# Optimization experiments

Hardware: AMD Instinct MI355X
Metric: run time of the kernel (lower is better)

The kernel has to match this reference:

```python
import jax, jax.numpy as jnp
import numpy as np

B, C, H, W, K = 2, 64, 192, 192, 7
PAD = K // 2
EPS = 1e-6


def _win_idx(L):
    # NATTEN border handling: window is shifted (not zero-padded) to stay in-bounds.
    i = jnp.arange(L)
    start = jnp.clip(i - PAD, 0, L - K)            # [L] window start per query pos
    win = start[:, None] + jnp.arange(K)[None]     # [L,K] absolute key positions
    pb = (K - 1) - (i - start)                     # [L] rpb start index per query pos
    pbi = pb[:, None] + jnp.arange(K)[None]        # [L,K] rpb table indices
    return win, pbi


def setup_inputs() -> dict:
    key = jax.random.key(0)
    ks = jax.random.split(key, 10)
    g = jax.random.normal(ks[0], (B, C, H, W), jnp.float32)
    cd = jax.random.uniform(ks[1], (B, 1, H, W), dtype=jnp.float32)
    dense = jax.random.uniform(ks[2], (B, 1, H, W), dtype=jnp.float32)
    sel = jax.random.uniform(ks[3], (B, 1, H, W)) < 0.05
    sd = jnp.where(sel, dense, 0.0)
    mask = (jax.random.uniform(ks[4], (B, 1, H, W)) < 0.5).astype(jnp.float32)
    ln_w = 1.0 + 0.02 * jax.random.normal(ks[5], (C,), jnp.float32)
    ln_b = 0.02 * jax.random.normal(ks[6], (C,), jnp.float32)
    conv_w = 0.05 * jax.random.normal(ks[7], (2 * C, C + 1), jnp.float32)  # 1x1 conv
    conv_b = 0.02 * jax.random.normal(ks[8], (2 * C,), jnp.float32)
    rpb = 0.02 * jax.random.normal(ks[9], (1, 2 * K - 1, 2 * K - 1), jnp.float32)
    return {"g": g, "cd": cd, "sd": sd, "mask": mask,
            "ln_w": ln_w, "ln_b": ln_b, "conv_w": conv_w, "conv_b": conv_b, "rpb": rpb}


def reference(g, cd, sd, mask, ln_w, ln_b, conv_w, conv_b, rpb):
    # LayerNorm2d: normalize over channel dim per spatial location
    mu = g.mean(axis=1, keepdims=True)
    var = ((g - mu) ** 2).mean(axis=1, keepdims=True)
    gn = (g - mu) * jax.lax.rsqrt(var + EPS)
    gn = gn * ln_w[None, :, None, None] + ln_b[None, :, None, None]

    z = jnp.concatenate([gn, cd], axis=1)                      # [B,C+1,H,W]
    qk = jnp.einsum('bchw,oc->bohw', z, conv_w) + conv_b[None, :, None, None]
    q, k = qk[:, :C], qk[:, C:]
    k = k * mask

    qc = q.transpose(0, 2, 3, 1)                               # [B,H,W,C] single head
    kc = k.transpose(0, 2, 3, 1)
    rwin, rpbi = _win_idx(H)
    cwin, cpbi = _win_idx(W)

    # NATTEN qk + relative position bias over 7x7 neighborhoods
    k_win = kc[:, rwin][:, :, :, cwin]                         # [B,H,K,W,K,C]
    attn = jnp.einsum('bhwc,bhiwjc->bhwij', qc, k_win)         # [B,H,W,K,K]
    bias = rpb[0][rpbi][:, :, cpbi]                            # [H,K,W,K]
    attn = attn + bias.transpose(0, 2, 1, 3)[None]
    a = jax.nn.softmax(attn.reshape(B, H, W, K * K), axis=-1).reshape(B, H, W, K, K)

    # NATTEN av with v = cd (head_dim 1)
    v_win = cd[:, 0][:, rwin][:, :, :, cwin]                   # [B,H,K,W,K]
    cd_out = jnp.einsum('bhwij,bhiwj->bhw', a, v_win)[:, None]  # [B,1,H,W]
    m_win = mask[:, 0][:, rwin][:, :, :, cwin]
    mask_out = jnp.einsum('bhwij,bhiwj->bhw', a, m_win)[:, None]

    # NYU / SDR post-processing
    cd_out = cd_out * mask + cd * (1.0 - mask)
    valid = sd > 0
    cd_out = jnp.where(valid, sd, cd_out)
    mask_out = jnp.where(valid, mask, mask_out)
    return cd_out, mask_out
```

## Files before the change

kernel.cpp:

```cpp
#include <hip/hip_runtime.h>

constexpr int NB = 2;
constexpr int NC = 64;
constexpr int NH = 192;
constexpr int NW = 192;
constexpr int NK = 7;
constexpr int NHW = NH * NW;
constexpr int NPIX = NB * NHW;
constexpr float EPS = 1e-6f;

__global__ __launch_bounds__(256) void qk_gemm(
    const float* __restrict__ g, const float* __restrict__ cd,
    const float* __restrict__ mask,
    const float* __restrict__ ln_w, const float* __restrict__ ln_b,
    const float* __restrict__ conv_w, const float* __restrict__ conv_b,
    float* __restrict__ qbuf, float* __restrict__ kbuf)
{
    __shared__ float Z[65][128];
    __shared__ float WTc[33][128];

    int tid = threadIdx.x;
    int p0 = blockIdx.x * 128;
    int b  = p0 / NHW;
    int hw0 = p0 - b * NHW;

    int px = tid >> 1;
    int hf = tid & 1;
    const float* gp = g + (size_t)(b * NC + hf * 32) * NHW + (hw0 + px);
    float vals[32];
    float s = 0.f, sq = 0.f;
#pragma unroll
    for (int j = 0; j < 32; ++j) {
        float v = gp[(size_t)j * NHW];
        vals[j] = v; s += v; sq += v * v;
    }
    s  += __shfl_xor(s, 1);
    sq += __shfl_xor(sq, 1);
    float mu   = s * (1.f / 64.f);
    float rstd = rsqrtf(sq * (1.f / 64.f) - mu * mu + EPS);
#pragma unroll
    for (int j = 0; j < 32; ++j) {
        int c = hf * 32 + j;
        Z[c][px] = (vals[j] - mu) * rstd * ln_w[c] + ln_b[c];
    }
    if (hf) Z[64][px] = cd[p0 + px];

    int og = tid >> 4;
    int pg = tid & 15;
    float acc[8][8];
#pragma unroll
    for (int oi = 0; oi < 8; ++oi)
#pragma unroll
        for (int pj = 0; pj < 8; ++pj) acc[oi][pj] = 0.f;

    for (int cc = 0; cc < 65; cc += 33) {
        int nr = (65 - cc < 33) ? (65 - cc) : 33;
        __syncthreads();
        if (tid < 128) {
            int o = tid;
            for (int r = 0; r < nr; ++r)
                WTc[r][o] = conv_w[o * 65 + cc + r];
        }
        __syncthreads();
        for (int r = 0; r < nr; ++r) {
            float4 w0 = *(const float4*)&WTc[r][8 * og];
            float4 w1 = *(const float4*)&WTc[r][8 * og + 4];
            float4 z0 = *(const float4*)&Z[cc + r][8 * pg];
            float4 z1 = *(const float4*)&Z[cc + r][8 * pg + 4];
            float w8[8] = {w0.x, w0.y, w0.z, w0.w, w1.x, w1.y, w1.z, w1.w};
            float z8[8] = {z0.x, z0.y, z0.z, z0.w, z1.x, z1.y, z1.z, z1.w};
#pragma unroll
            for (int oi = 0; oi < 8; ++oi)
#pragma unroll
                for (int pj = 0; pj < 8; ++pj)
                    acc[oi][pj] = fmaf(w8[oi], z8[pj], acc[oi][pj]);
        }
    }

    int o0  = og * 8;
    int pxb = pg * 8;
    float4 ba = *(const float4*)&conv_b[o0];
    float4 bb = *(const float4*)&conv_b[o0 + 4];
    float bia[8] = {ba.x, ba.y, ba.z, ba.w, bb.x, bb.y, bb.z, bb.w};
    bool isq = (o0 < 64);
    float m8[8];
    if (!isq) {
        float4 ma = *(const float4*)&mask[p0 + pxb];
        float4 mc = *(const float4*)&mask[p0 + pxb + 4];
        m8[0]=ma.x; m8[1]=ma.y; m8[2]=ma.z; m8[3]=ma.w;
        m8[4]=mc.x; m8[5]=mc.y; m8[6]=mc.z; m8[7]=mc.w;
    }
    float* base = isq ? (qbuf + (size_t)(b * NC + o0) * NHW + hw0 + pxb)
                      : (kbuf + (size_t)(b * NC + o0 - 64) * NHW + hw0 + pxb);
#pragma unroll
    for (int oi = 0; oi < 8; ++oi) {
        float v[8];
#pragma unroll
        for (int pj = 0; pj < 8; ++pj) {
            float t = acc[oi][pj] + bia[oi];
            v[pj] = isq ? t : t * m8[pj];
        }
        float* dst = base + (size_t)oi * NHW;
        *(float4*)&dst[0] = make_float4(v[0], v[1], v[2], v[3]);
        *(float4*)&dst[4] = make_float4(v[4], v[5], v[6], v[7]);
    }
}

__global__ __launch_bounds__(256) void attn_tile(
    const float* __restrict__ qbuf, const float* __restrict__ kbuf,
    const float* __restrict__ cd, const float* __restrict__ sd,
    const float* __restrict__ mask, const float* __restrict__ rpb,
    float* __restrict__ out_cd, float* __restrict__ out_mask)
{
    __shared__ float kst[4][2][10 * 24];
    __shared__ float cdt[14 * 24];
    __shared__ float mt [14 * 24];
    __shared__ float rpbt[169];
    __shared__ float xch[128][49];

    int tid  = threadIdx.x;
    int g    = tid >> 6;
    int lane = tid & 63;
    int rq   = g & 1;
    int half = g >> 1;
    int tx   = lane & 15;
    int tyw  = lane >> 4;

    int bw = blockIdx.x % 12;
    int t2 = blockIdx.x / 12;
    int bh = t2 % 24;
    int b  = t2 / 24;
    int w0 = bw * 16, h0 = bh * 8;
    int hr0 = h0 + rq * 4;

    int h = hr0 + tyw;
    int w = w0 + tx;
    int rs = min(max(h - 3, 0), NH - NK);
    int cs = min(max(w - 3, 0), NW - NK);
    int rb  = (rs - (hr0 - 3)) * 24 + (cs - (w0 - 3));
    int rbB = (rs - (h0  - 3)) * 24 + (cs - (w0 - 3));

    const float* cdb = cd   + (size_t)b * NHW;
    const float* msb = mask + (size_t)b * NHW;
    for (int e = tid; e < 308; e += 256) {
        int r = e / 22, c2 = e - r * 22;
        int gr = min(max(h0 - 3 + r, 0), NH - 1);
        int gc = min(max(w0 - 3 + c2, 0), NW - 1);
        cdt[r * 24 + c2] = cdb[gr * NW + gc];
        mt [r * 24 + c2] = msb[gr * NW + gc];
    }
    if (tid < 169) rpbt[tid] = rpb[tid];

    int soff[4], slds[4]; bool sact[4];
#pragma unroll
    for (int s = 0; s < 4; ++s) {
        int e = lane + 64 * s;
        int r = e / 22, c2 = e - r * 22;
        int gr = min(max(hr0 - 3 + r, 0), NH - 1);
        int gc = min(max(w0 - 3 + c2, 0), NW - 1);
        soff[s] = gr * NW + gc;
        slds[s] = r * 24 + c2;
        sact[s] = (e < 220);
    }

    const float* kb = kbuf + (size_t)(b * NC + half * 32) * NHW;
    const float* qb = qbuf + (size_t)(b * NC + half * 32) * NHW + h * NW + w;

    float at[49];
#pragma unroll
    for (int n = 0; n < 49; ++n) at[n] = 0.f;

    float st[4];
#pragma unroll
    for (int s = 0; s < 4; ++s) st[s] = sact[s] ? kb[soff[s]] : 0.f;
    float* k0 = kst[g][0];
    float* k1 = kst[g][1];
#pragma unroll
    for (int s = 0; s < 4; ++s) if (sact[s]) k0[slds[s]] = st[s];

    for (int i = 0; i < 32; ++i) {
        if (i + 1 < 32) {
            const float* kb2 = kb + (size_t)(i + 1) * NHW;
#pragma unroll
            for (int s = 0; s < 4; ++s) st[s] = sact[s] ? kb2[soff[s]] : 0.f;
        }
        float q = qb[(size_t)i * NHW];
        const float* kt = ((i & 1) ? k1 : k0) + rb;
#pragma unroll
        for (int r = 0; r < 7; ++r)
#pragma unroll
            for (int j = 0; j < 7; ++j)
                at[r * 7 + j] = fmaf(q, kt[r * 24 + j], at[r * 7 + j]);
        if (i + 1 < 32) {
            float* nk = (i & 1) ? k0 : k1;
#pragma unroll
            for (int s = 0; s < 4; ++s) if (sact[s]) nk[slds[s]] = st[s];
        }
    }

    int pxid = (rq * 4 + tyw) * 16 + tx;
    __syncthreads();
    if (half == 1) {
#pragma unroll
        for (int n = 0; n < 49; ++n) xch[pxid][n] = at[n];
    }
    __syncthreads();
    int pr = 6 - (h - rs);
    int pc = 6 - (w - cs);
    if (half == 0) {
#pragma unroll
        for (int n = 0; n < 49; ++n) at[n] += xch[pxid][n];
#pragma unroll
        for (int r = 0; r < 7; ++r)
#pragma unroll
            for (int j = 0; j < 7; ++j)
                at[r * 7 + j] += rpbt[(pr + r) * 13 + pc + j];
#pragma unroll
        for (int n = 0; n < 49; ++n) xch[pxid][n] = at[n];
    }
    __syncthreads();
    if (half == 1) {
#pragma unroll
        for (int n = 0; n < 49; ++n) at[n] = xch[pxid][n];
    }

    float mx = -1e30f;
#pragma unroll
    for (int n = 0; n < 49; ++n) mx = fmaxf(mx, at[n]);
    float sm = 0.f;
#pragma unroll
    for (int n = 0; n < 49; ++n) {
        at[n] = __expf(at[n] - mx);
        sm += at[n];
    }

    const float* vt = (half ? mt : cdt) + rbB;
    float sv = 0.f;
#pragma unroll
    for (int r = 0; r < 7; ++r)
#pragma unroll
        for (int j = 0; j < 7; ++j)
            sv = fmaf(at[r * 7 + j], vt[r * 24 + j], sv);
    sv /= sm;

    int p = b * NHW + h * NW + w;
    float sdc = sd[p];
    int cidx = (rq * 4 + tyw + 3) * 24 + (tx + 3);
    float mc = mt[cidx];
    if (half == 0) {
        float cdc = cdt[cidx];
        float co = sv * mc + cdc * (1.f - mc);
        if (sdc > 0.f) co = sdc;
        out_cd[p] = co;
    } else {
        out_mask[p] = (sdc > 0.f) ? mc : sv;
    }
}

extern "C" void kernel_launch(void* const* d_in, const int* in_sizes, int n_in,
                              void* d_out, int out_size, void* d_ws, size_t ws_size,
                              hipStream_t stream) {
    const float* g      = (const float*)d_in[0];
    const float* cd     = (const float*)d_in[1];
    const float* sd     = (const float*)d_in[2];
    const float* mask   = (const float*)d_in[3];
    const float* ln_w   = (const float*)d_in[4];
    const float* ln_b   = (const float*)d_in[5];
    const float* conv_w = (const float*)d_in[6];
    const float* conv_b = (const float*)d_in[7];
    const float* rpb    = (const float*)d_in[8];

    float* out  = (float*)d_out;
    float* qbuf = (float*)d_ws;
    float* kbuf = qbuf + (size_t)NB * NC * NHW;

    qk_gemm<<<dim3(NPIX / 128), dim3(256), 0, stream>>>(
        g, cd, mask, ln_w, ln_b, conv_w, conv_b, qbuf, kbuf);
    attn_tile<<<dim3(NB * 24 * 12), dim3(256), 0, stream>>>(
        qbuf, kbuf, cd, sd, mask, rpb, out, out + NPIX);
}
```

Before: 141.7 us.

## Interleave q/k channels in groups of four and load float4 in attention

```diff
diff --git a/kernel.cpp b/kernel.cpp
--- a/kernel.cpp
+++ b/kernel.cpp
@@ -9,12 +9,13 @@
 constexpr int NPIX = NB * NHW;
 constexpr float EPS = 1e-6f;
 
+
 __global__ __launch_bounds__(256) void qk_gemm(
     const float* __restrict__ g, const float* __restrict__ cd,
     const float* __restrict__ mask,
     const float* __restrict__ ln_w, const float* __restrict__ ln_b,
     const float* __restrict__ conv_w, const float* __restrict__ conv_b,
-    float* __restrict__ qbuf, float* __restrict__ kbuf)
+    float* __restrict__ qk)
 {
     __shared__ float Z[65][128];
     __shared__ float WTc[33][128];
@@ -90,33 +91,33 @@
         m8[0]=ma.x; m8[1]=ma.y; m8[2]=ma.z; m8[3]=ma.w;
         m8[4]=mc.x; m8[5]=mc.y; m8[6]=mc.z; m8[7]=mc.w;
     }
-    float* base = isq ? (qbuf + (size_t)(b * NC + o0) * NHW + hw0 + pxb)
-                      : (kbuf + (size_t)(b * NC + o0 - 64) * NHW + hw0 + pxb);
-#pragma unroll
-    for (int oi = 0; oi < 8; ++oi) {
-        float v[8];
+#pragma unroll
+    for (int qd = 0; qd < 2; ++qd) {
+        int grp = (o0 >> 2) + qd;
+        float* dst = qk + ((size_t)(b * 32 + grp) * NHW + hw0 + pxb) * 4;
 #pragma unroll
         for (int pj = 0; pj < 8; ++pj) {
-            float t = acc[oi][pj] + bia[oi];
-            v[pj] = isq ? t : t * m8[pj];
-        }
-        float* dst = base + (size_t)oi * NHW;
-        *(float4*)&dst[0] = make_float4(v[0], v[1], v[2], v[3]);
-        *(float4*)&dst[4] = make_float4(v[4], v[5], v[6], v[7]);
+            float vv[4];
+#pragma unroll
+            for (int ci = 0; ci < 4; ++ci) {
+                float tv = acc[qd * 4 + ci][pj] + bia[qd * 4 + ci];
+                vv[ci] = isq ? tv : tv * m8[pj];
+            }
+            *(float4*)(dst + pj * 4) = make_float4(vv[0], vv[1], vv[2], vv[3]);
+        }
     }
 }
 
 __global__ __launch_bounds__(256) void attn_tile(
-    const float* __restrict__ qbuf, const float* __restrict__ kbuf,
+    const float* __restrict__ qk,
     const float* __restrict__ cd, const float* __restrict__ sd,
     const float* __restrict__ mask, const float* __restrict__ rpb,
     float* __restrict__ out_cd, float* __restrict__ out_mask)
 {
-    __shared__ float kst[4][2][10 * 24];
-    __shared__ float cdt[14 * 24];
-    __shared__ float mt [14 * 24];
-    __shared__ float rpbt[169];
-    __shared__ float xch[128][49];
+    __shared__ float smem[7680 + 336 + 336 + 169];
+    float* cdt  = smem + 7680;
+    float* mt   = smem + 7680 + 336;
+    float* rpbt = smem + 7680 + 672;
 
     int tid  = threadIdx.x;
     int g    = tid >> 6;
@@ -126,8 +127,10 @@
     int tx   = lane & 15;
     int tyw  = lane >> 4;
 
-    int bw = blockIdx.x % 12;
-    int t2 = blockIdx.x / 12;
+    int bid = blockIdx.x;
+    int swz = (bid & 7) * 72 + (bid >> 3);
+    int bw = swz % 12;
+    int t2 = swz / 12;
     int bh = t2 % 24;
     int b  = t2 / 24;
     int w0 = bw * 16, h0 = bh * 8;
@@ -158,46 +161,69 @@
         int r = e / 22, c2 = e - r * 22;
         int gr = min(max(hr0 - 3 + r, 0), NH - 1);
         int gc = min(max(w0 - 3 + c2, 0), NW - 1);
-        soff[s] = gr * NW + gc;
+        soff[s] = (gr * NW + gc) * 4;
         slds[s] = r * 24 + c2;
         sact[s] = (e < 220);
     }
 
-    const float* kb = kbuf + (size_t)(b * NC + half * 32) * NHW;
-    const float* qb = qbuf + (size_t)(b * NC + half * 32) * NHW + h * NW + w;
+    const float* kb0 = qk + (size_t)(b * 32 + 16 + half * 8) * NHW * 4;
+    const float* qb0 = qk + ((size_t)(b * 32 + half * 8) * NHW + h * NW + w) * 4;
+
+    float* kw = smem + g * 1920;
 
     float at[49];
 #pragma unroll
     for (int n = 0; n < 49; ++n) at[n] = 0.f;
 
-    float st[4];
-#pragma unroll
-    for (int s = 0; s < 4; ++s) st[s] = sact[s] ? kb[soff[s]] : 0.f;
-    float* k0 = kst[g][0];
-    float* k1 = kst[g][1];
-#pragma unroll
-    for (int s = 0; s < 4; ++s) if (sact[s]) k0[slds[s]] = st[s];
-
-    for (int i = 0; i < 32; ++i) {
-        if (i + 1 < 32) {
-            const float* kb2 = kb + (size_t)(i + 1) * NHW;
-#pragma unroll
-            for (int s = 0; s < 4; ++s) st[s] = sact[s] ? kb2[soff[s]] : 0.f;
-        }
-        float q = qb[(size_t)i * NHW];
-        const float* kt = ((i & 1) ? k1 : k0) + rb;
-#pragma unroll
-        for (int r = 0; r < 7; ++r)
-#pragma unroll
-            for (int j = 0; j < 7; ++j)
-                at[r * 7 + j] = fmaf(q, kt[r * 24 + j], at[r * 7 + j]);
-        if (i + 1 < 32) {
-            float* nk = (i & 1) ? k0 : k1;
-#pragma unroll
-            for (int s = 0; s < 4; ++s) if (sact[s]) nk[slds[s]] = st[s];
-        }
-    }
-
+    float4 stg[4];
+    float4 qn;
+#pragma unroll
+    for (int s = 0; s < 4; ++s)
+        stg[s] = sact[s] ? *(const float4*)(kb0 + soff[s])
+                         : make_float4(0.f, 0.f, 0.f, 0.f);
+    qn = *(const float4*)qb0;
+#pragma unroll
+    for (int s = 0; s < 4; ++s) if (sact[s]) {
+        kw[0 * 240 + slds[s]] = stg[s].x;
+        kw[1 * 240 + slds[s]] = stg[s].y;
+        kw[2 * 240 + slds[s]] = stg[s].z;
+        kw[3 * 240 + slds[s]] = stg[s].w;
+    }
+
+    for (int t = 0; t < 8; ++t) {
+        float4 qv = qn;
+        if (t < 7) {
+            const float* kbn = kb0 + (size_t)(t + 1) * (NHW * 4);
+#pragma unroll
+            for (int s = 0; s < 4; ++s)
+                if (sact[s]) stg[s] = *(const float4*)(kbn + soff[s]);
+            qn = *(const float4*)(qb0 + (size_t)(t + 1) * (NHW * 4));
+        }
+        const float* kbuf = kw + (t & 1) * 960;
+#pragma unroll
+        for (int ccq = 0; ccq < 4; ++ccq) {
+            float q = (ccq == 0) ? qv.x : (ccq == 1) ? qv.y
+                    : (ccq == 2) ? qv.z : qv.w;
+            const float* kt = kbuf + ccq * 240 + rb;
+#pragma unroll
+            for (int r = 0; r < 7; ++r)
+#pragma unroll
+                for (int j = 0; j < 7; ++j)
+                    at[r * 7 + j] = fmaf(q, kt[r * 24 + j], at[r * 7 + j]);
+        }
+        if (t < 7) {
+            float* nk = kw + ((t + 1) & 1) * 960;
+#pragma unroll
+            for (int s = 0; s < 4; ++s) if (sact[s]) {
+                nk[0 * 240 + slds[s]] = stg[s].x;
+                nk[1 * 240 + slds[s]] = stg[s].y;
+                nk[2 * 240 + slds[s]] = stg[s].z;
+                nk[3 * 240 + slds[s]] = stg[s].w;
+            }
+        }
+    }
+
+    float (*xch)[49] = (float(*)[49])smem;
     int pxid = (rq * 4 + tyw) * 16 + tx;
     __syncthreads();
     if (half == 1) {
@@ -270,12 +296,11 @@
     const float* conv_b = (const float*)d_in[7];
     const float* rpb    = (const float*)d_in[8];
 
-    float* out  = (float*)d_out;
-    float* qbuf = (float*)d_ws;
-    float* kbuf = qbuf + (size_t)NB * NC * NHW;
+    float* out   = (float*)d_out;
+    float* qkbuf = (float*)d_ws;
 
     qk_gemm<<<dim3(NPIX / 128), dim3(256), 0, stream>>>(
-        g, cd, mask, ln_w, ln_b, conv_w, conv_b, qbuf, kbuf);
+        g, cd, mask, ln_w, ln_b, conv_w, conv_b, qkbuf);
     attn_tile<<<dim3(NB * 24 * 12), dim3(256), 0, stream>>>(
-        qbuf, kbuf, cd, sd, mask, rpb, out, out + NPIX);
+        qkbuf, cd, sd, mask, rpb, out, out + NPIX);
 }
```

After: 158.0 us. 1.12x slower.

## Deepen K-channel prefetch to 4-stage LDS ring and swizzle block order

Applied to the files above, without the earlier changes.

```diff
diff --git a/kernel.cpp b/kernel.cpp
--- a/kernel.cpp
+++ b/kernel.cpp
@@ -112,7 +112,7 @@
     const float* __restrict__ mask, const float* __restrict__ rpb,
     float* __restrict__ out_cd, float* __restrict__ out_mask)
 {
-    __shared__ float kst[4][2][10 * 24];
+    __shared__ float kst[4][4][240];
     __shared__ float cdt[14 * 24];
     __shared__ float mt [14 * 24];
     __shared__ float rpbt[169];
@@ -126,8 +126,10 @@
     int tx   = lane & 15;
     int tyw  = lane >> 4;
 
-    int bw = blockIdx.x % 12;
-    int t2 = blockIdx.x / 12;
+    int bid = blockIdx.x;
+    int swz = (bid & 7) * 72 + (bid >> 3);
+    int bw = swz % 12;
+    int t2 = swz / 12;
     int bh = t2 % 24;
     int b  = t2 / 24;
     int w0 = bw * 16, h0 = bh * 8;
@@ -170,32 +172,48 @@
 #pragma unroll
     for (int n = 0; n < 49; ++n) at[n] = 0.f;
 
-    float st[4];
-#pragma unroll
-    for (int s = 0; s < 4; ++s) st[s] = sact[s] ? kb[soff[s]] : 0.f;
-    float* k0 = kst[g][0];
-    float* k1 = kst[g][1];
-#pragma unroll
-    for (int s = 0; s < 4; ++s) if (sact[s]) k0[slds[s]] = st[s];
-
+    float* kw = &kst[g][0][0];
+
+    float st0[4], st1[4], stC[4];
+#pragma unroll
+    for (int s = 0; s < 4; ++s) st0[s] = sact[s] ? kb[soff[s]] : 0.f;
+#pragma unroll
+    for (int s = 0; s < 4; ++s) st1[s] = sact[s] ? kb[NHW + soff[s]] : 0.f;
+#pragma unroll
+    for (int s = 0; s < 4; ++s) stC[s] = sact[s] ? kb[2 * NHW + soff[s]] : 0.f;
+    float qA = qb[0];
+    float qB = qb[NHW];
+    float qC = qb[2 * (size_t)NHW];
+#pragma unroll
+    for (int s = 0; s < 4; ++s) if (sact[s]) kw[0 * 240 + slds[s]] = st0[s];
+#pragma unroll
+    for (int s = 0; s < 4; ++s) if (sact[s]) kw[1 * 240 + slds[s]] = st1[s];
+
+#pragma unroll 4
     for (int i = 0; i < 32; ++i) {
-        if (i + 1 < 32) {
-            const float* kb2 = kb + (size_t)(i + 1) * NHW;
-#pragma unroll
-            for (int s = 0; s < 4; ++s) st[s] = sact[s] ? kb2[soff[s]] : 0.f;
-        }
-        float q = qb[(size_t)i * NHW];
-        const float* kt = ((i & 1) ? k1 : k0) + rb;
+        float stN[4]; float qN;
+        if (i + 3 < 32) {
+            const float* kbn = kb + (size_t)(i + 3) * NHW;
+#pragma unroll
+            for (int s = 0; s < 4; ++s)
+                if (sact[s]) stN[s] = kbn[soff[s]];
+            qN = qb[(size_t)(i + 3) * NHW];
+        }
+        const float* kt = kw + (i & 3) * 240 + rb;
+        float q = qA;
 #pragma unroll
         for (int r = 0; r < 7; ++r)
 #pragma unroll
             for (int j = 0; j < 7; ++j)
                 at[r * 7 + j] = fmaf(q, kt[r * 24 + j], at[r * 7 + j]);
-        if (i + 1 < 32) {
-            float* nk = (i & 1) ? k0 : k1;
-#pragma unroll
-            for (int s = 0; s < 4; ++s) if (sact[s]) nk[slds[s]] = st[s];
-        }
+        if (i + 2 < 32) {
+            float* nk = kw + ((i + 2) & 3) * 240;
+#pragma unroll
+            for (int s = 0; s < 4; ++s) if (sact[s]) nk[slds[s]] = stC[s];
+        }
+#pragma unroll
+        for (int s = 0; s < 4; ++s) stC[s] = stN[s];
+        qA = qB; qB = qC; qC = qN;
     }
 
     int pxid = (rq * 4 + tyw) * 16 + tx;
```

Measured after the change: 156.4 us. 10.4% more time.

## Split attention channel reduction across four wave pairs with 512-thread blocks

Applied to the files above, without the earlier changes.

```diff
diff --git a/kernel.cpp b/kernel.cpp
--- a/kernel.cpp
+++ b/kernel.cpp
@@ -106,13 +106,13 @@
     }
 }
 
-__global__ __launch_bounds__(256) void attn_tile(
+__global__ __launch_bounds__(512) void attn_tile(
     const float* __restrict__ qbuf, const float* __restrict__ kbuf,
     const float* __restrict__ cd, const float* __restrict__ sd,
     const float* __restrict__ mask, const float* __restrict__ rpb,
     float* __restrict__ out_cd, float* __restrict__ out_mask)
 {
-    __shared__ float kst[4][2][10 * 24];
+    __shared__ float kst[8][2][240];
     __shared__ float cdt[14 * 24];
     __shared__ float mt [14 * 24];
     __shared__ float rpbt[169];
@@ -122,12 +122,14 @@
     int g    = tid >> 6;
     int lane = tid & 63;
     int rq   = g & 1;
-    int half = g >> 1;
+    int quar = g >> 1;
     int tx   = lane & 15;
     int tyw  = lane >> 4;
 
-    int bw = blockIdx.x % 12;
-    int t2 = blockIdx.x / 12;
+    int bid = blockIdx.x;
+    int swz = (bid & 7) * 72 + (bid >> 3);
+    int bw = swz % 12;
+    int t2 = swz / 12;
     int bh = t2 % 24;
     int b  = t2 / 24;
     int w0 = bw * 16, h0 = bh * 8;
@@ -142,7 +144,7 @@
 
     const float* cdb = cd   + (size_t)b * NHW;
     const float* msb = mask + (size_t)b * NHW;
-    for (int e = tid; e < 308; e += 256) {
+    for (int e = tid; e < 308; e += 512) {
         int r = e / 22, c2 = e - r * 22;
         int gr = min(max(h0 - 3 + r, 0), NH - 1);
         int gc = min(max(w0 - 3 + c2, 0), NW - 1);
@@ -163,8 +165,8 @@
         sact[s] = (e < 220);
     }
 
-    const float* kb = kbuf + (size_t)(b * NC + half * 32) * NHW;
-    const float* qb = qbuf + (size_t)(b * NC + half * 32) * NHW + h * NW + w;
+    const float* kb = kbuf + (size_t)(b * NC + quar * 16) * NHW;
+    const float* qb = qbuf + (size_t)(b * NC + quar * 16) * NHW + h * NW + w;
 
     float at[49];
 #pragma unroll
@@ -177,21 +179,25 @@
     float* k1 = kst[g][1];
 #pragma unroll
     for (int s = 0; s < 4; ++s) if (sact[s]) k0[slds[s]] = st[s];
-
-    for (int i = 0; i < 32; ++i) {
-        if (i + 1 < 32) {
+    float qA = qb[0];
+    float qB = qb[NHW];
+
+    for (int i = 0; i < 16; ++i) {
+        if (i + 1 < 16) {
             const float* kb2 = kb + (size_t)(i + 1) * NHW;
 #pragma unroll
             for (int s = 0; s < 4; ++s) st[s] = sact[s] ? kb2[soff[s]] : 0.f;
         }
-        float q = qb[(size_t)i * NHW];
+        float q = qA;
+        qA = qB;
+        if (i + 2 < 16) qB = qb[(size_t)(i + 2) * NHW];
         const float* kt = ((i & 1) ? k1 : k0) + rb;
 #pragma unroll
         for (int r = 0; r < 7; ++r)
 #pragma unroll
             for (int j = 0; j < 7; ++j)
                 at[r * 7 + j] = fmaf(q, kt[r * 24 + j], at[r * 7 + j]);
-        if (i + 1 < 32) {
+        if (i + 1 < 16) {
             float* nk = (i & 1) ? k0 : k1;
 #pragma unroll
             for (int s = 0; s < 4; ++s) if (sact[s]) nk[slds[s]] = st[s];
@@ -199,15 +205,24 @@
     }
 
     int pxid = (rq * 4 + tyw) * 16 + tx;
-    __syncthreads();
-    if (half == 1) {
+    if (quar == 3) {
 #pragma unroll
         for (int n = 0; n < 49; ++n) xch[pxid][n] = at[n];
+    }
+    __syncthreads();
+    if (quar == 2) {
+#pragma unroll
+        for (int n = 0; n < 49; ++n) xch[pxid][n] += at[n];
+    }
+    __syncthreads();
+    if (quar == 1) {
+#pragma unroll
+        for (int n = 0; n < 49; ++n) xch[pxid][n] += at[n];
     }
     __syncthreads();
     int pr = 6 - (h - rs);
     int pc = 6 - (w - cs);
-    if (half == 0) {
+    if (quar == 0) {
 #pragma unroll
         for (int n = 0; n < 49; ++n) at[n] += xch[pxid][n];
 #pragma unroll
@@ -219,7 +234,8 @@
         for (int n = 0; n < 49; ++n) xch[pxid][n] = at[n];
     }
     __syncthreads();
-    if (half == 1) {
+    if (quar >= 2) return;
+    if (quar == 1) {
 #pragma unroll
         for (int n = 0; n < 49; ++n) at[n] = xch[pxid][n];
     }
@@ -234,7 +250,7 @@
         sm += at[n];
     }
 
-    const float* vt = (half ? mt : cdt) + rbB;
+    const float* vt = (quar ? mt : cdt) + rbB;
     float sv = 0.f;
 #pragma unroll
     for (int r = 0; r < 7; ++r)
@@ -247,7 +263,7 @@
     float sdc = sd[p];
     int cidx = (rq * 4 + tyw + 3) * 24 + (tx + 3);
     float mc = mt[cidx];
-    if (half == 0) {
+    if (quar == 0) {
         float cdc = cdt[cidx];
         float co = sv * mc + cdc * (1.f - mc);
         if (sdc > 0.f) co = sdc;
@@ -276,6 +292,6 @@
 
     qk_gemm<<<dim3(NPIX / 128), dim3(256), 0, stream>>>(
         g, cd, mask, ln_w, ln_b, conv_w, conv_b, qbuf, kbuf);
-    attn_tile<<<dim3(NB * 24 * 12), dim3(256), 0, stream>>>(
+    attn_tile<<<dim3(NB * 24 * 12), dim3(512), 0, stream>>>(
         qbuf, kbuf, cd, sd, mask, rpb, out, out + NPIX);
 }
```

Measured after the change: 147.5 us. 1.04x slower.
